# Optimization experiments

Measured on AMD Instinct MI355X. Metric: run time of the kernel, lower is better.

The kernel has to match this reference:

```python
import jax, jax.numpy as jnp
import numpy as np

B, N, C = 8, 1024, 768
H, D = 12, 64  # num_heads, head_dim; C == H*D
SCALE = 1.0 / np.sqrt(D)
NEG_INF = -1e9


def setup_inputs() -> dict:
    key = jax.random.key(0)
    k1, k2, k3, k4 = jax.random.split(key, 4)
    x = jax.random.normal(k1, (B, N, C), dtype=jnp.float32)
    # additive padding mask: 0 for valid tokens, -1e9 for padded tail
    lengths = jax.random.randint(k2, (B,), N // 2, N + 1)  # valid lengths per sample
    pad = jnp.arange(N)[None, :] >= lengths[:, None]       # [B, N] True = padded
    attn_mask = jnp.where(pad, NEG_INF, 0.0).astype(jnp.float32)[:, None, None, :]  # [B,1,1,N]
    W_qkv = jax.random.normal(k3, (C, 3 * C), dtype=jnp.float32) * (C ** -0.5)
    b_qkv = jnp.zeros((3 * C,), dtype=jnp.float32)
    W_proj = jax.random.normal(k4, (C, C), dtype=jnp.float32) * (C ** -0.5)
    b_proj = jnp.zeros((C,), dtype=jnp.float32)
    return {"x": x, "attn_mask": attn_mask, "W_qkv": W_qkv, "b_qkv": b_qkv,
            "W_proj": W_proj, "b_proj": b_proj}


def reference(x, attn_mask, W_qkv, b_qkv, W_proj, b_proj):
    qkv = (x @ W_qkv + b_qkv).reshape(B, N, 3, H, D)
    qkv = jnp.transpose(qkv, (2, 0, 3, 1, 4))
    q, k, v = qkv[0], qkv[1], qkv[2]
    attn = jnp.einsum('bhnd,bhmd->bhnm', q, k) * SCALE  # [B, H, N, N]
    attn = attn + attn_mask                              # broadcast [B,1,1,N]
    attn = jax.nn.softmax(attn, axis=-1)
    out = jnp.einsum('bhnm,bhmd->bhnd', attn, v)         # [B, H, N, D]
    out = jnp.transpose(out, (0, 2, 1, 3)).reshape(B, N, C)
    return out @ W_proj + b_proj
```

## Files before the change

kernel.cpp:

```cpp
#include <hip/hip_runtime.h>
#include <stdint.h>

#define NB 8
#define NHEAD 12
#define SEQ 1024
#define CDIM 768
#define HDIM 64

#define SCALE_L2E 0.1803368801111244f
#define L2E 1.4426950408889634f

typedef __attribute__((ext_vector_type(8))) short bf16x8;
typedef __attribute__((ext_vector_type(4))) short bf16x4;
typedef __attribute__((ext_vector_type(4))) float f32x4;
typedef __attribute__((ext_vector_type(4))) unsigned short us4;

__device__ __forceinline__ void gload_lds16(const void* g, void* l) {
  __builtin_amdgcn_global_load_lds((const __attribute__((address_space(1))) void*)g,
                                   (__attribute__((address_space(3))) void*)l,
                                   16, 0, 0);
}

__device__ __forceinline__ unsigned short f2bf(float f) {
  __bf16 h = (__bf16)f;
  return __builtin_bit_cast(unsigned short, h);
}

__device__ __forceinline__ f32x4 mfma16(bf16x8 a, bf16x8 b, f32x4 c) {
  return __builtin_amdgcn_mfma_f32_16x16x32_bf16(a, b, c, 0, 0, 0);
}

template <int N>
__device__ __forceinline__ void s_waitcnt_vm() {
  if constexpr (N == 0) asm volatile("s_waitcnt vmcnt(0)" ::: "memory");
  else if constexpr (N == 4) asm volatile("s_waitcnt vmcnt(4)" ::: "memory");
  else if constexpr (N == 8) asm volatile("s_waitcnt vmcnt(8)" ::: "memory");
  else static_assert(N == 0, "unsupported vmcnt literal");
}


__global__ void cvt_x_kernel(const float* __restrict__ in,
                             unsigned short* __restrict__ out, int n8) {
  int i = blockIdx.x * blockDim.x + threadIdx.x;
  if (i >= n8) return;
  const float4* p = (const float4*)in;
  float4 a = p[2 * i], b = p[2 * i + 1];
  union { bf16x8 v; unsigned short h[8]; } u;
  u.h[0] = f2bf(a.x); u.h[1] = f2bf(a.y); u.h[2] = f2bf(a.z); u.h[3] = f2bf(a.w);
  u.h[4] = f2bf(b.x); u.h[5] = f2bf(b.y); u.h[6] = f2bf(b.z); u.h[7] = f2bf(b.w);
  ((bf16x8*)out)[i] = u.v;
}

__global__ void tconv_kernel(const float* __restrict__ in,
                             unsigned short* __restrict__ out, int K, int N) {
  __shared__ float tile[32][33];
  int tx = threadIdx.x & 31, ty = threadIdx.x >> 5;
  int n0 = blockIdx.x * 32, k0 = blockIdx.y * 32;
#pragma unroll
  for (int i = 0; i < 4; i++)
    tile[ty + 8 * i][tx] = in[(size_t)(k0 + ty + 8 * i) * N + n0 + tx];
  __syncthreads();
#pragma unroll
  for (int i = 0; i < 4; i++)
    out[(size_t)(n0 + ty + 8 * i) * K + k0 + tx] = f2bf(tile[tx][ty + 8 * i]);
}

template <int BM, int BN, int EPI>
__global__ __launch_bounds__(256, EPI ? 4 : 2)
void gemm_bt_kernel(const unsigned short* __restrict__ A,
                    const unsigned short* __restrict__ Bt,
                    const float* __restrict__ bias,
                    unsigned short* __restrict__ q_out,
                    unsigned short* __restrict__ k_out,
                    unsigned short* __restrict__ v_out,
                    float* __restrict__ f_out,
                    int M, int N, int K) {
  constexpr int WM = BM / 2, WN = BN / 2;
  constexpr int MI = WM / 16, NJ = WN / 16;
  constexpr int CA = BM / 32, CB = BN / 32;
  constexpr int LOADS = CA + CB;
  __shared__ __align__(16) unsigned short As[2][BM * 64];
  __shared__ __align__(16) unsigned short Bs[2][BN * 64];
  const int t = threadIdx.x;
  const int w = t >> 6, l = t & 63;
  const int g = l >> 4, lr = l & 15;
  const int wr = w >> 1, wc = w & 1;
  const int nTN = N / BN;
  const int bpx = gridDim.x >> 3;
  const int orig = (blockIdx.x & 7) * bpx + (blockIdx.x >> 3);
  const int bm = orig / nTN, bn = orig % nTN;
  const int m0 = bm * BM, n0 = bn * BN;

  f32x4 acc[MI][NJ];
#pragma unroll
  for (int i = 0; i < MI; i++)
#pragma unroll
    for (int j = 0; j < NJ; j++) acc[i][j] = f32x4{0.f, 0.f, 0.f, 0.f};

  const unsigned short* aP[CA];
  const unsigned short* bP[CB];
#pragma unroll
  for (int i = 0; i < CA; i++) {
    int c = t + 256 * i, r = c >> 3, s = c & 7;
    aP[i] = A + (size_t)(m0 + r) * K + (s ^ (r & 7)) * 8;
  }
#pragma unroll
  for (int i = 0; i < CB; i++) {
    int c = t + 256 * i, r = c >> 3, s = c & 7;
    bP[i] = Bt + (size_t)(n0 + r) * K + (s ^ (r & 7)) * 8;
  }

  auto stage = [&](int buf, int kk) {
#pragma unroll
    for (int i = 0; i < CA; i++)
      gload_lds16(aP[i] + kk, As[buf] + (t + 256 * i) * 8);
#pragma unroll
    for (int i = 0; i < CB; i++)
      gload_lds16(bP[i] + kk, Bs[buf] + (t + 256 * i) * 8);
  };

  stage(0, 0);
  const int nt = K >> 6;
  for (int tt = 0; tt < nt; ++tt) {
    const int cur = tt & 1;
    if (tt + 1 < nt) {
      stage(cur ^ 1, (tt + 1) << 6);
      s_waitcnt_vm<LOADS>();
    } else {
      s_waitcnt_vm<0>();
    }
    __builtin_amdgcn_sched_barrier(0);
    __builtin_amdgcn_s_barrier();
    const unsigned short* Ab = As[cur];
    const unsigned short* Bb = Bs[cur];
#pragma unroll
    for (int ks = 0; ks < 2; ks++) {
      const int slot = ((ks * 4 + g) ^ (lr & 7)) << 3;
      bf16x8 af[MI];
#pragma unroll
      for (int i = 0; i < MI; i++) {
        int row = wr * WM + i * 16 + lr;
        af[i] = *(const bf16x8*)(Ab + row * 64 + slot);
      }
#pragma unroll
      for (int j = 0; j < NJ; j++) {
        int row = wc * WN + j * 16 + lr;
        bf16x8 bfr = *(const bf16x8*)(Bb + row * 64 + slot);
#pragma unroll
        for (int i = 0; i < MI; i++) acc[i][j] = mfma16(af[i], bfr, acc[i][j]);
      }
    }
    asm volatile("" ::: "memory");
    __builtin_amdgcn_s_barrier();
    __builtin_amdgcn_sched_barrier(0);
  }

  float bv[NJ];
#pragma unroll
  for (int j = 0; j < NJ; j++) bv[j] = bias[n0 + wc * WN + j * 16 + lr];

  if (EPI == 1) {
#pragma unroll
    for (int i = 0; i < MI; i++) {
      int mrow = m0 + wr * WM + i * 16 + 4 * g;
#pragma unroll
      for (int j = 0; j < NJ; j++) {
        int n = n0 + wc * WN + j * 16 + lr;
#pragma unroll
        for (int r = 0; r < 4; r++)
          f_out[(size_t)(mrow + r) * N + n] = acc[i][j][r] + bv[j];
      }
    }
  } else {
    const int which = n0 / CDIM;
    const int bb = m0 / SEQ;
    const int tok0 = (m0 % SEQ) + wr * WM;
#pragma unroll
    for (int j = 0; j < NJ; j++) {
      int ncol = (n0 % CDIM) + wc * WN + j * 16;
      int hh = ncol / 64;
      int d = (ncol % 64) + lr;
#pragma unroll
      for (int i = 0; i < MI; i++) {
        int tokb = tok0 + i * 16 + 4 * g;
        if (which == 2) {
          us4 pk;
#pragma unroll
          for (int r = 0; r < 4; r++) pk[r] = f2bf(acc[i][j][r] + bv[j]);
          *(us4*)(v_out + ((size_t)(bb * NHEAD + hh) * 64 + d) * SEQ + tokb) = pk;
        } else {
          unsigned short* dst = (which == 0) ? q_out : k_out;
#pragma unroll
          for (int r = 0; r < 4; r++)
            dst[((size_t)(bb * NHEAD + hh) * SEQ + tokb + r) * 64 + d] =
                f2bf(acc[i][j][r] + bv[j]);
        }
      }
    }
  }
}

__global__ __launch_bounds__(256, 3)
void attn_kernel(const unsigned short* __restrict__ Qb,
                 const unsigned short* __restrict__ Kb,
                 const unsigned short* __restrict__ Vt,
                 const float* __restrict__ mask,
                 unsigned short* __restrict__ Ob) {
  __shared__ __align__(16) unsigned short Qs[128 * 64];
  __shared__ __align__(16) unsigned short Ks[128 * 64];
  __shared__ __align__(16) unsigned short Vs[64 * 128];
  __shared__ __align__(16) float smask[128];

  const int hwb = blockIdx.x;
  const int x = hwb & 7;
  const int i = hwb >> 3;
  const int qt = i & 7;
  const int bh = (i >> 3) * 8 + x;
  const int h = bh % NHEAD, b = bh / NHEAD;

  const int t = threadIdx.x, w = t >> 6, l = t & 63;
  const int g = l >> 4, lr = l & 15;

  const unsigned short* Qg = Qb + (((size_t)b * NHEAD + h) * SEQ + qt * 128) * 64;
  const unsigned short* Kg = Kb + ((size_t)b * NHEAD + h) * SEQ * 64;
  const unsigned short* Vg = Vt + ((size_t)b * NHEAD + h) * 64 * SEQ;
  const float* mg = mask + (size_t)b * SEQ;

  int nkb = 8;
#pragma unroll
  for (int kb = 7; kb >= 4; kb--)
    if (mg[kb * 128] < -1e8f) nkb = kb;

  bf16x8 kreg[4], vreg[4];
  float mreg;
  auto prefetch = [&](int kb) {
#pragma unroll
    for (int ii = 0; ii < 4; ii++) {
      int c = t + 256 * ii;
      int rk = c >> 3, sk = c & 7;
      kreg[ii] = *(const bf16x8*)(Kg + (size_t)(kb * 128 + rk) * 64 +
                                  ((sk ^ (rk & 7)) << 3));
      int rv = c >> 4, sv = c & 15;
      vreg[ii] = *(const bf16x8*)(Vg + (size_t)rv * SEQ + kb * 128 +
                                  ((sv ^ (rv & 15)) << 3));
    }
    mreg = (t < 128) ? mg[kb * 128 + t] * L2E : 0.f;
  };
  auto commit = [&]() {
#pragma unroll
    for (int ii = 0; ii < 4; ii++) {
      *(bf16x8*)(Ks + (t + 256 * ii) * 8) = kreg[ii];
      *(bf16x8*)(Vs + (t + 256 * ii) * 8) = vreg[ii];
    }
    if (t < 128) smask[t] = mreg;
  };

#pragma unroll
  for (int ii = 0; ii < 4; ii++) {
    int c = t + 256 * ii;
    int row = c >> 3, sl = c & 7;
    gload_lds16(Qg + row * 64 + ((sl ^ (row & 7)) << 3), Qs + c * 8);
  }
  prefetch(0);
  __syncthreads();

  bf16x8 qfr[2][2];
#pragma unroll
  for (int qi = 0; qi < 2; qi++)
#pragma unroll
    for (int ks = 0; ks < 2; ks++) {
      int row = w * 32 + qi * 16 + lr;
      qfr[qi][ks] =
          *(const bf16x8*)(Qs + row * 64 + (((ks * 4 + g) ^ (lr & 7)) << 3));
    }

  float l_run[2] = {0.f, 0.f};
  f32x4 oacc[2][4];
#pragma unroll
  for (int qi = 0; qi < 2; qi++)
#pragma unroll
    for (int df = 0; df < 4; df++) oacc[qi][df] = f32x4{0.f, 0.f, 0.f, 0.f};

  for (int kb = 0; kb < nkb; kb++) {
    __syncthreads();
    commit();
    __syncthreads();
    if (kb + 1 < nkb) prefetch(kb + 1);

    float bs[2] = {0.f, 0.f};
    bf16x8 pa[4][2];
#pragma unroll
    for (int kc = 0; kc < 4; kc++) {
      f32x4 s0[2], s1[2];
#pragma unroll
      for (int qi = 0; qi < 2; qi++) {
        s0[qi] = f32x4{0.f, 0.f, 0.f, 0.f};
        s1[qi] = f32x4{0.f, 0.f, 0.f, 0.f};
      }
#pragma unroll
      for (int ks = 0; ks < 2; ks++) {
        int row0 = (2 * kc) * 16 + lr;
        int row1 = (2 * kc + 1) * 16 + lr;
        int slot = ((ks * 4 + g) ^ (lr & 7)) << 3;
        bf16x8 a0 = *(const bf16x8*)(Ks + row0 * 64 + slot);
        bf16x8 a1 = *(const bf16x8*)(Ks + row1 * 64 + slot);
        s0[0] = mfma16(a0, qfr[0][ks], s0[0]);
        s0[1] = mfma16(a0, qfr[1][ks], s0[1]);
        s1[0] = mfma16(a1, qfr[0][ks], s1[0]);
        s1[1] = mfma16(a1, qfr[1][ks], s1[1]);
      }
      f32x4 mv0 = *(const f32x4*)(smask + (2 * kc) * 16 + 4 * g);
      f32x4 mv1 = *(const f32x4*)(smask + (2 * kc + 1) * 16 + 4 * g);
#pragma unroll
      for (int qi = 0; qi < 2; qi++) {
        union { bf16x8 v; unsigned short hh[8]; } u;
#pragma unroll
        for (int r = 0; r < 4; r++) {
          float p0 = __builtin_amdgcn_exp2f(fmaf(s0[qi][r], SCALE_L2E, mv0[r]));
          float p1 = __builtin_amdgcn_exp2f(fmaf(s1[qi][r], SCALE_L2E, mv1[r]));
          bs[qi] += p0 + p1;
          u.hh[r] = f2bf(p0);
          u.hh[4 + r] = f2bf(p1);
        }
        pa[kc][qi] = u.v;
      }
    }
    bs[0] += __shfl_xor(bs[0], 16);
    bs[0] += __shfl_xor(bs[0], 32);
    bs[1] += __shfl_xor(bs[1], 16);
    bs[1] += __shfl_xor(bs[1], 32);
    l_run[0] += bs[0];
    l_run[1] += bs[1];

#pragma unroll
    for (int kc = 0; kc < 4; kc++) {
      const int c16lo = kc * 4 + (g >> 1);
      const int odd = (g & 1) << 3;
#pragma unroll
      for (int df = 0; df < 4; df++) {
        const char* vp = (const char*)(Vs + (df * 16 + lr) * 128);
        bf16x4 lo = *(const bf16x4*)(vp + (((c16lo ^ lr) << 4) | odd));
        bf16x4 hi = *(const bf16x4*)(vp + ((((c16lo + 2) ^ lr) << 4) | odd));
        bf16x8 vb = __builtin_shufflevector(lo, hi, 0, 1, 2, 3, 4, 5, 6, 7);
        oacc[0][df] = mfma16(pa[kc][0], vb, oacc[0][df]);
        oacc[1][df] = mfma16(pa[kc][1], vb, oacc[1][df]);
      }
    }
  }

#pragma unroll
  for (int qi = 0; qi < 2; qi++) {
    float linv = 1.f / l_run[qi];
#pragma unroll
    for (int r = 0; r < 4; r++) {
      float li = __shfl(linv, 4 * g + r);
      int tok = qt * 128 + w * 32 + qi * 16 + 4 * g + r;
#pragma unroll
      for (int df = 0; df < 4; df++) {
        float val = oacc[qi][df][r] * li;
        Ob[((size_t)b * SEQ + tok) * CDIM + h * 64 + df * 16 + lr] = f2bf(val);
      }
    }
  }
}

extern "C" void kernel_launch(void* const* d_in, const int* in_sizes, int n_in,
                              void* d_out, int out_size, void* d_ws,
                              size_t ws_size, hipStream_t stream) {
  const float* x = (const float*)d_in[0];
  const float* mask = (const float*)d_in[1];
  const float* Wqkv = (const float*)d_in[2];
  const float* bqkv = (const float*)d_in[3];
  const float* Wproj = (const float*)d_in[4];
  const float* bproj = (const float*)d_in[5];
  float* out = (float*)d_out;

  char* ws = (char*)d_ws;
  size_t off = 0;
  auto take = [&](size_t bytes) {
    char* p = ws + off;
    off += (bytes + 255) & ~(size_t)255;
    return p;
  };
  unsigned short* xb = (unsigned short*)take((size_t)NB * SEQ * CDIM * 2);
  unsigned short* wqt = (unsigned short*)take((size_t)3 * CDIM * CDIM * 2);
  unsigned short* wpt = (unsigned short*)take((size_t)CDIM * CDIM * 2);
  unsigned short* Qb = (unsigned short*)take((size_t)NB * NHEAD * SEQ * 64 * 2);
  unsigned short* Kbf = (unsigned short*)take((size_t)NB * NHEAD * SEQ * 64 * 2);
  unsigned short* Vt = (unsigned short*)take((size_t)NB * NHEAD * SEQ * 64 * 2);
  unsigned short* Ob = (unsigned short*)take((size_t)NB * SEQ * CDIM * 2);

  int n8 = NB * SEQ * CDIM / 8;
  cvt_x_kernel<<<(n8 + 255) / 256, 256, 0, stream>>>(x, xb, n8);
  tconv_kernel<<<dim3(3 * CDIM / 32, CDIM / 32), 256, 0, stream>>>(Wqkv, wqt,
                                                                   CDIM, 3 * CDIM);
  tconv_kernel<<<dim3(CDIM / 32, CDIM / 32), 256, 0, stream>>>(Wproj, wpt, CDIM,
                                                               CDIM);
  gemm_bt_kernel<128, 128, 0>
      <<<(NB * SEQ / 128) * (3 * CDIM / 128), 256, 0, stream>>>(
          xb, wqt, bqkv, Qb, Kbf, Vt, nullptr, NB * SEQ, 3 * CDIM, CDIM);
  attn_kernel<<<NB * NHEAD * 8, 256, 0, stream>>>(Qb, Kbf, Vt, mask, Ob);
  gemm_bt_kernel<64, 64, 1>
      <<<(NB * SEQ / 64) * (CDIM / 64), 256, 0, stream>>>(
          Ob, wpt, bproj, nullptr, nullptr, nullptr, out, NB * SEQ, CDIM, CDIM);
}
```

Baseline: 203.3 us.

## Merge prep kernels into one launch and use BK=32 tiles for QKV GEMM

Folds the x-to-bf16 conversion and the two weight transpose-conversions into a single prep kernel, which removes two kernel launches and the gaps between them. The GEMM kernel gains a BK template parameter with a matching LDS swizzle for 32-wide K tiles. The QKV GEMM switches to BK=32 with launch bounds of 4 waves, which halves its LDS footprint so more blocks fit per CU. The cost is twice as many K iterations and barriers, plus a new swizzle pattern whose bank-conflict behaviour is untested.

```diff
diff --git a/kernel.cpp b/kernel.cpp
--- a/kernel.cpp
+++ b/kernel.cpp
@@ -38,24 +38,17 @@
   else static_assert(N == 0, "unsupported vmcnt literal");
 }
 
-
-__global__ void cvt_x_kernel(const float* __restrict__ in,
-                             unsigned short* __restrict__ out, int n8) {
-  int i = blockIdx.x * blockDim.x + threadIdx.x;
-  if (i >= n8) return;
-  const float4* p = (const float4*)in;
-  float4 a = p[2 * i], b = p[2 * i + 1];
-  union { bf16x8 v; unsigned short h[8]; } u;
-  u.h[0] = f2bf(a.x); u.h[1] = f2bf(a.y); u.h[2] = f2bf(a.z); u.h[3] = f2bf(a.w);
-  u.h[4] = f2bf(b.x); u.h[5] = f2bf(b.y); u.h[6] = f2bf(b.z); u.h[7] = f2bf(b.w);
-  ((bf16x8*)out)[i] = u.v;
-}
-
-__global__ void tconv_kernel(const float* __restrict__ in,
-                             unsigned short* __restrict__ out, int K, int N) {
-  __shared__ float tile[32][33];
-  int tx = threadIdx.x & 31, ty = threadIdx.x >> 5;
-  int n0 = blockIdx.x * 32, k0 = blockIdx.y * 32;
+#define CVT_BLOCKS 3072
+#define T1_BLOCKS 1728
+#define T2_BLOCKS 576
+#define PREP_BLOCKS (CVT_BLOCKS + T1_BLOCKS + T2_BLOCKS)
+
+__device__ __forceinline__ void tconv_body(const float* __restrict__ in,
+                                           unsigned short* __restrict__ out,
+                                           int K, int N, int bx, int by, int t,
+                                           float (*tile)[33]) {
+  int tx = t & 31, ty = t >> 5;
+  int n0 = bx * 32, k0 = by * 32;
 #pragma unroll
   for (int i = 0; i < 4; i++)
     tile[ty + 8 * i][tx] = in[(size_t)(k0 + ty + 8 * i) * N + n0 + tx];
@@ -65,8 +58,33 @@
     out[(size_t)(n0 + ty + 8 * i) * K + k0 + tx] = f2bf(tile[tx][ty + 8 * i]);
 }
 
-template <int BM, int BN, int EPI>
-__global__ __launch_bounds__(256, EPI ? 4 : 2)
+__global__ void prep_kernel(const float* __restrict__ x,
+                            const float* __restrict__ Wqkv,
+                            const float* __restrict__ Wproj,
+                            unsigned short* __restrict__ xb,
+                            unsigned short* __restrict__ wqt,
+                            unsigned short* __restrict__ wpt) {
+  __shared__ float tile[32][33];
+  const int blk = blockIdx.x, t = threadIdx.x;
+  if (blk < CVT_BLOCKS) {
+    int i = blk * 256 + t;
+    const float4* p = (const float4*)x;
+    float4 a = p[2 * i], b = p[2 * i + 1];
+    union { bf16x8 v; unsigned short h[8]; } u;
+    u.h[0] = f2bf(a.x); u.h[1] = f2bf(a.y); u.h[2] = f2bf(a.z); u.h[3] = f2bf(a.w);
+    u.h[4] = f2bf(b.x); u.h[5] = f2bf(b.y); u.h[6] = f2bf(b.z); u.h[7] = f2bf(b.w);
+    ((bf16x8*)xb)[i] = u.v;
+  } else if (blk < CVT_BLOCKS + T1_BLOCKS) {
+    int bi = blk - CVT_BLOCKS;
+    tconv_body(Wqkv, wqt, CDIM, 3 * CDIM, bi % (3 * CDIM / 32), bi / (3 * CDIM / 32), t, tile);
+  } else {
+    int bi = blk - CVT_BLOCKS - T1_BLOCKS;
+    tconv_body(Wproj, wpt, CDIM, CDIM, bi % (CDIM / 32), bi / (CDIM / 32), t, tile);
+  }
+}
+
+template <int BM, int BN, int BK, int EPI>
+__global__ __launch_bounds__(256, 4)
 void gemm_bt_kernel(const unsigned short* __restrict__ A,
                     const unsigned short* __restrict__ Bt,
                     const float* __restrict__ bias,
@@ -77,10 +95,12 @@
                     int M, int N, int K) {
   constexpr int WM = BM / 2, WN = BN / 2;
   constexpr int MI = WM / 16, NJ = WN / 16;
-  constexpr int CA = BM / 32, CB = BN / 32;
+  constexpr int S = BK / 8;
+  constexpr int CA = BM * BK / 2048;
+  constexpr int CB = BN * BK / 2048;
   constexpr int LOADS = CA + CB;
-  __shared__ __align__(16) unsigned short As[2][BM * 64];
-  __shared__ __align__(16) unsigned short Bs[2][BN * 64];
+  __shared__ __align__(16) unsigned short As[2][BM * BK];
+  __shared__ __align__(16) unsigned short Bs[2][BN * BK];
   const int t = threadIdx.x;
   const int w = t >> 6, l = t & 63;
   const int g = l >> 4, lr = l & 15;
@@ -101,13 +121,15 @@
   const unsigned short* bP[CB];
 #pragma unroll
   for (int i = 0; i < CA; i++) {
-    int c = t + 256 * i, r = c >> 3, s = c & 7;
-    aP[i] = A + (size_t)(m0 + r) * K + (s ^ (r & 7)) * 8;
+    int c = t + 256 * i, r = c / S, s = c % S;
+    int kc = (S == 8) ? (s ^ (r & 7)) : (s ^ ((r >> 1) & 3));
+    aP[i] = A + (size_t)(m0 + r) * K + kc * 8;
   }
 #pragma unroll
   for (int i = 0; i < CB; i++) {
-    int c = t + 256 * i, r = c >> 3, s = c & 7;
-    bP[i] = Bt + (size_t)(n0 + r) * K + (s ^ (r & 7)) * 8;
+    int c = t + 256 * i, r = c / S, s = c % S;
+    int kc = (S == 8) ? (s ^ (r & 7)) : (s ^ ((r >> 1) & 3));
+    bP[i] = Bt + (size_t)(n0 + r) * K + kc * 8;
   }
 
   auto stage = [&](int buf, int kk) {
@@ -119,12 +141,14 @@
       gload_lds16(bP[i] + kk, Bs[buf] + (t + 256 * i) * 8);
   };
 
+  const int rswz = (S == 8) ? (lr & 7) : ((lr >> 1) & 3);
+
   stage(0, 0);
-  const int nt = K >> 6;
+  const int nt = K / BK;
   for (int tt = 0; tt < nt; ++tt) {
     const int cur = tt & 1;
     if (tt + 1 < nt) {
-      stage(cur ^ 1, (tt + 1) << 6);
+      stage(cur ^ 1, (tt + 1) * BK);
       s_waitcnt_vm<LOADS>();
     } else {
       s_waitcnt_vm<0>();
@@ -134,18 +158,18 @@
     const unsigned short* Ab = As[cur];
     const unsigned short* Bb = Bs[cur];
 #pragma unroll
-    for (int ks = 0; ks < 2; ks++) {
-      const int slot = ((ks * 4 + g) ^ (lr & 7)) << 3;
+    for (int ks = 0; ks < BK / 32; ks++) {
+      const int slot = ((ks * 4 + g) ^ rswz) << 3;
       bf16x8 af[MI];
 #pragma unroll
       for (int i = 0; i < MI; i++) {
         int row = wr * WM + i * 16 + lr;
-        af[i] = *(const bf16x8*)(Ab + row * 64 + slot);
+        af[i] = *(const bf16x8*)(Ab + row * BK + slot);
       }
 #pragma unroll
       for (int j = 0; j < NJ; j++) {
         int row = wc * WN + j * 16 + lr;
-        bf16x8 bfr = *(const bf16x8*)(Bb + row * 64 + slot);
+        bf16x8 bfr = *(const bf16x8*)(Bb + row * BK + slot);
 #pragma unroll
         for (int i = 0; i < MI; i++) acc[i][j] = mfma16(af[i], bfr, acc[i][j]);
       }
@@ -390,17 +414,12 @@
   unsigned short* Vt = (unsigned short*)take((size_t)NB * NHEAD * SEQ * 64 * 2);
   unsigned short* Ob = (unsigned short*)take((size_t)NB * SEQ * CDIM * 2);
 
-  int n8 = NB * SEQ * CDIM / 8;
-  cvt_x_kernel<<<(n8 + 255) / 256, 256, 0, stream>>>(x, xb, n8);
-  tconv_kernel<<<dim3(3 * CDIM / 32, CDIM / 32), 256, 0, stream>>>(Wqkv, wqt,
-                                                                   CDIM, 3 * CDIM);
-  tconv_kernel<<<dim3(CDIM / 32, CDIM / 32), 256, 0, stream>>>(Wproj, wpt, CDIM,
-                                                               CDIM);
-  gemm_bt_kernel<128, 128, 0>
+  prep_kernel<<<PREP_BLOCKS, 256, 0, stream>>>(x, Wqkv, Wproj, xb, wqt, wpt);
+  gemm_bt_kernel<128, 128, 32, 0>
       <<<(NB * SEQ / 128) * (3 * CDIM / 128), 256, 0, stream>>>(
           xb, wqt, bqkv, Qb, Kbf, Vt, nullptr, NB * SEQ, 3 * CDIM, CDIM);
   attn_kernel<<<NB * NHEAD * 8, 256, 0, stream>>>(Qb, Kbf, Vt, mask, Ob);
-  gemm_bt_kernel<64, 64, 1>
+  gemm_bt_kernel<64, 64, 64, 1>
       <<<(NB * SEQ / 64) * (CDIM / 64), 256, 0, stream>>>(
           Ob, wpt, bproj, nullptr, nullptr, nullptr, out, NB * SEQ, CDIM, CDIM);
 }
```

After: 199.4 us. No clear change (-1.9%).
